# Kernel optimization log

Measured on AMD Instinct MI355X. Metric: run time of the kernel, lower is better.

## Reference

```python
import jax, jax.numpy as jnp
import numpy as np


def setup_inputs() -> dict:
    key = jax.random.key(0)
    k1, k2, k3, k4 = jax.random.split(key, 4)
    N, M, d = 512, 4096, 8
    return {
        "X": jax.random.normal(k1, (N, M), jnp.float32),
        "C_tilde": jax.random.normal(k2, (d, N), jnp.float32),
        "S_tilde": jax.random.normal(k3, (N, d), jnp.float32),
        "tau_tilde": jax.random.normal(k4, (N, d), jnp.float32),
    }


def reference(X, C_tilde, S_tilde, tau_tilde):
    # X: [N, M] real; C_tilde: [d, N]; S_tilde, tau_tilde: [N, d]
    N, M = X.shape
    f = jnp.arange(M, dtype=X.dtype) / M                         # [M]
    # omega[N,d,M] = exp(-2*pi*i * tau[N,d] * f[M])
    phase = tau_tilde[:, :, None] * f                            # [N, d, M] real
    omega = jnp.exp((-2j * jnp.pi) * phase.astype(jnp.complex64))  # [N, d, M] complex64

    X_F = jnp.fft.fft(X)                                         # [N, M] complex64
    X_F_align = X_F[:, None, :] * jnp.conj(omega)                # [N, d, M]

    C = jax.nn.softmax(C_tilde, axis=1).astype(jnp.complex64)    # [d, N]
    A_F = jnp.einsum('dN,NdM->dM', C, X_F_align)                 # [d, M]

    S = jax.nn.softmax(S_tilde, axis=1).astype(jnp.complex64)    # [N, d]
    # S_shift[N,d,M] = S[N,d] * omega[N,d,M]; x = sum_d S_shift * A_F
    x = jnp.einsum('Nd,NdM,dM->NM', S, omega, A_F)               # [N, M] complex64
    return x
```

## Files before the change

### kernel.cpp

```cpp
#include <hip/hip_runtime.h>
#include <math.h>

#define N_ROWS 512
#define M_LEN  4096
#define D_DIM  8
#define NCHUNK 8

__device__ __forceinline__ float2 f2(float x, float y) { return make_float2(x, y); }
__device__ __forceinline__ float2 cmul(float2 a, float2 b){
  return f2(a.x*b.x - a.y*b.y, a.x*b.y + a.y*b.x);
}
__device__ __forceinline__ float2 cadd(float2 a, float2 b){ return f2(a.x+b.x, a.y+b.y); }
__device__ __forceinline__ float2 csub(float2 a, float2 b){ return f2(a.x-b.x, a.y-b.y); }
__device__ __forceinline__ int ph(int i){ return i + (i>>4) + (i>>8); }
__device__ __forceinline__ int dr6(int j){
  int r = 0;
  #pragma unroll
  for (int i = 0; i < 6; ++i){ r = (r<<2) | (j & 3); j >>= 2; }
  return r;
}

static constexpr float TWO_PI = 6.283185307179586476925f;

__global__ __launch_bounds__(256) void softmax_kernel(
    const float* __restrict__ Ct, const float* __restrict__ St,
    float* __restrict__ C, float* __restrict__ S) {
  int b = blockIdx.x, tid = threadIdx.x;
  if (b < D_DIM) {
    __shared__ float red[256];
    const float* row = Ct + b * N_ROWS;
    float v0 = row[tid], v1 = row[tid + 256];
    float mx = fmaxf(v0, v1);
    red[tid] = mx; __syncthreads();
    for (int s = 128; s > 0; s >>= 1) {
      if (tid < s) red[tid] = fmaxf(red[tid], red[tid + s]);
      __syncthreads();
    }
    float m = red[0];
    __syncthreads();
    float e0 = __expf(v0 - m), e1 = __expf(v1 - m);
    red[tid] = e0 + e1; __syncthreads();
    for (int s = 128; s > 0; s >>= 1) {
      if (tid < s) red[tid] += red[tid + s];
      __syncthreads();
    }
    float inv = 1.0f / red[0];
    C[b * N_ROWS + tid]       = e0 * inv;
    C[b * N_ROWS + tid + 256] = e1 * inv;
  } else {
    int n = (b - D_DIM) * 256 + tid;
    if (n < N_ROWS) {
      float v[D_DIM];
      float mx = -3.0e38f;
      #pragma unroll
      for (int d = 0; d < D_DIM; ++d) { v[d] = St[n * D_DIM + d]; mx = fmaxf(mx, v[d]); }
      float sum = 0.f;
      #pragma unroll
      for (int d = 0; d < D_DIM; ++d) { v[d] = __expf(v[d] - mx); sum += v[d]; }
      float inv = 1.0f / sum;
      #pragma unroll
      for (int d = 0; d < D_DIM; ++d) S[n * D_DIM + d] = v[d] * inv;
    }
  }
}

__global__ __launch_bounds__(256) void fft_kernel(
    const float* __restrict__ X, float2* __restrict__ XF) {
  __shared__ float2 buf[4368];
  int row = blockIdx.x;
  int tid = threadIdx.x;
  const float* x = X + (size_t)row * M_LEN;
  for (int j = tid; j < M_LEN; j += 256)
    buf[ph(dr6(j))] = f2(x[j], 0.0f);
  __syncthreads();
  for (int s = 0; s < 6; ++s) {
    int quarter = 1 << (2*s);
    float angf = -TWO_PI / (float)(quarter << 2);
    for (int bi = tid; bi < 1024; bi += 256) {
      int k  = bi & (quarter - 1);
      int g  = bi >> (2*s);
      int i0 = (g << (2*s + 2)) + k;
      float sw, cw; __sincosf(angf * (float)k, &sw, &cw);
      float2 w1 = f2(cw, sw);
      float2 w2 = cmul(w1, w1);
      float2 w3 = cmul(w2, w1);
      float2 a0 = buf[ph(i0)];
      float2 a1 = cmul(buf[ph(i0 +   quarter)], w1);
      float2 a2 = cmul(buf[ph(i0 + 2*quarter)], w2);
      float2 a3 = cmul(buf[ph(i0 + 3*quarter)], w3);
      float2 t0 = cadd(a0, a2), t1 = csub(a0, a2);
      float2 t2 = cadd(a1, a3), t3 = csub(a1, a3);
      buf[ph(i0)]             = cadd(t0, t2);
      buf[ph(i0 +   quarter)] = f2(t1.x + t3.y, t1.y - t3.x);
      buf[ph(i0 + 2*quarter)] = csub(t0, t2);
      buf[ph(i0 + 3*quarter)] = f2(t1.x - t3.y, t1.y + t3.x);
    }
    __syncthreads();
  }
  for (int j = tid; j < M_LEN; j += 256)
    XF[(size_t)row * M_LEN + j] = buf[ph(j)];
}

__global__ __launch_bounds__(256) void zero_af_kernel(float4* __restrict__ AF) {
  int i = blockIdx.x * 256 + threadIdx.x;
  if (i < (D_DIM * M_LEN) / 2)
    AF[i] = make_float4(0.f, 0.f, 0.f, 0.f);
}

__global__ __launch_bounds__(256) void af_kernel(
    const float2* __restrict__ XF, const float* __restrict__ C,
    const float* __restrict__ tau, float* __restrict__ AF) {
  int bid   = blockIdx.x;
  int chunk = bid >> 7;
  int idx   = (bid & 127) * 256 + threadIdx.x;
  int d = idx >> 12;
  int m = idx & (M_LEN - 1);
  float fm = (float)m * (1.0f / (float)M_LEN);
  float accr = 0.f, acci = 0.f;
  int n0 = chunk * (N_ROWS / NCHUNK);
  #pragma unroll 8
  for (int nn = 0; nn < N_ROWS / NCHUNK; ++nn) {
    int n = n0 + nn;
    float c = C[d * N_ROWS + n];
    float t = tau[n * D_DIM + d];
    float sa, ca;
    __sincosf(TWO_PI * t * fm, &sa, &ca);
    float2 Xv = XF[(size_t)n * M_LEN + m];
    accr += c * (Xv.x * ca - Xv.y * sa);
    acci += c * (Xv.x * sa + Xv.y * ca);
  }
  if (idx < D_DIM * M_LEN) {
    atomicAdd(&AF[2 * idx],     accr);
    atomicAdd(&AF[2 * idx + 1], acci);
  }
}

__global__ __launch_bounds__(256) void out_kernel(
    const float2* __restrict__ AF, const float* __restrict__ S,
    const float* __restrict__ tau, float* __restrict__ out, int interleaved) {
  int idx = blockIdx.x * 256 + threadIdx.x;
  int n = idx >> 12;
  int m = idx & (M_LEN - 1);
  float fm = (float)m * (1.0f / (float)M_LEN);
  float xr = 0.f, xi = 0.f;
  #pragma unroll
  for (int d = 0; d < D_DIM; ++d) {
    float s = S[n * D_DIM + d];
    float t = tau[n * D_DIM + d];
    float sa, ca;
    __sincosf(TWO_PI * t * fm, &sa, &ca);
    float2 A = AF[(d << 12) + m];
    xr += s * (ca * A.x + sa * A.y);
    xi += s * (ca * A.y - sa * A.x);
  }
  if (interleaved) {
    ((float2*)out)[idx] = f2(xr, xi);
  } else {
    out[idx] = xr;
  }
}

extern "C" void kernel_launch(void* const* d_in, const int* in_sizes, int n_in,
                              void* d_out, int out_size, void* d_ws, size_t ws_size,
                              hipStream_t stream) {
  const float* X  = (const float*)d_in[0];
  const float* Ct = (const float*)d_in[1];
  const float* St = (const float*)d_in[2];
  const float* tau= (const float*)d_in[3];

  char* ws = (char*)d_ws;
  const size_t XF_BYTES = (size_t)N_ROWS * M_LEN * sizeof(float2);
  const size_t AF_BYTES = (size_t)D_DIM * M_LEN * sizeof(float2);
  const size_t C_BYTES  = (size_t)D_DIM * N_ROWS * sizeof(float);
  float2* XF = (float2*)ws;
  float2* AF = (float2*)(ws + XF_BYTES);
  float*  C  = (float*)(ws + XF_BYTES + AF_BYTES);
  float*  S  = (float*)(ws + XF_BYTES + AF_BYTES + C_BYTES);

  int interleaved = (out_size >= 2 * N_ROWS * M_LEN) ? 1 : 0;

  softmax_kernel<<<D_DIM + (N_ROWS + 255) / 256, 256, 0, stream>>>(Ct, St, C, S);
  fft_kernel<<<N_ROWS, 256, 0, stream>>>(X, XF);
  zero_af_kernel<<<(D_DIM * M_LEN / 2 + 255) / 256, 256, 0, stream>>>((float4*)AF);
  af_kernel<<<NCHUNK * 128, 256, 0, stream>>>(XF, C, tau, (float*)AF);
  out_kernel<<<(N_ROWS * M_LEN) / 256, 256, 0, stream>>>(AF, S, tau, (float*)d_out, interleaved);
}
```

Before: 115.2 us.

## Reuse XF loads across all d in af_kernel and use revolution-based hardware sin/cos

The A_F accumulation now has each thread own one frequency m and keep 8 accumulators, one per d. Each XF element is therefore loaded once per n instead of once per (n,d), which cuts global traffic on the large XF buffer by a factor of eight. The N split grows from 8 to 32 chunks so the grid still fills the device, at the cost of more atomics. All sin/cos calls switch to AMD's native v_sin/v_cos builtins, which take angles in revolutions, so the 2*pi multiply and range reduction are dropped. The risk is lower accuracy for large arguments.

```diff
diff --git a/kernel.cpp b/kernel.cpp
--- a/kernel.cpp
+++ b/kernel.cpp
@@ -4,7 +4,7 @@
 #define N_ROWS 512
 #define M_LEN  4096
 #define D_DIM  8
-#define NCHUNK 8
+#define NCHUNK 32
 
 __device__ __forceinline__ float2 f2(float x, float y) { return make_float2(x, y); }
 __device__ __forceinline__ float2 cmul(float2 a, float2 b){
@@ -19,8 +19,8 @@
   for (int i = 0; i < 6; ++i){ r = (r<<2) | (j & 3); j >>= 2; }
   return r;
 }
-
-static constexpr float TWO_PI = 6.283185307179586476925f;
+__device__ __forceinline__ float sin_rev(float x){ return __builtin_amdgcn_sinf(x); }
+__device__ __forceinline__ float cos_rev(float x){ return __builtin_amdgcn_cosf(x); }
 
 __global__ __launch_bounds__(256) void softmax_kernel(
     const float* __restrict__ Ct, const float* __restrict__ St,
@@ -75,12 +75,13 @@
   __syncthreads();
   for (int s = 0; s < 6; ++s) {
     int quarter = 1 << (2*s);
-    float angf = -TWO_PI / (float)(quarter << 2);
+    float negInv = -1.0f / (float)(quarter << 2);
     for (int bi = tid; bi < 1024; bi += 256) {
       int k  = bi & (quarter - 1);
       int g  = bi >> (2*s);
       int i0 = (g << (2*s + 2)) + k;
-      float sw, cw; __sincosf(angf * (float)k, &sw, &cw);
+      float rev = negInv * (float)k;
+      float sw = sin_rev(rev), cw = cos_rev(rev);
       float2 w1 = f2(cw, sw);
       float2 w2 = cmul(w1, w1);
       float2 w3 = cmul(w2, w1);
@@ -111,27 +112,31 @@
     const float2* __restrict__ XF, const float* __restrict__ C,
     const float* __restrict__ tau, float* __restrict__ AF) {
   int bid   = blockIdx.x;
-  int chunk = bid >> 7;
-  int idx   = (bid & 127) * 256 + threadIdx.x;
-  int d = idx >> 12;
-  int m = idx & (M_LEN - 1);
-  float fm = (float)m * (1.0f / (float)M_LEN);
-  float accr = 0.f, acci = 0.f;
+  int chunk = bid >> 4;
+  int m     = (bid & 15) * 256 + threadIdx.x;
+  float fm  = (float)m * (1.0f / (float)M_LEN);
+  float accr[D_DIM], acci[D_DIM];
+  #pragma unroll
+  for (int d = 0; d < D_DIM; ++d) { accr[d] = 0.f; acci[d] = 0.f; }
   int n0 = chunk * (N_ROWS / NCHUNK);
-  #pragma unroll 8
+  #pragma unroll 4
   for (int nn = 0; nn < N_ROWS / NCHUNK; ++nn) {
     int n = n0 + nn;
-    float c = C[d * N_ROWS + n];
-    float t = tau[n * D_DIM + d];
-    float sa, ca;
-    __sincosf(TWO_PI * t * fm, &sa, &ca);
     float2 Xv = XF[(size_t)n * M_LEN + m];
-    accr += c * (Xv.x * ca - Xv.y * sa);
-    acci += c * (Xv.x * sa + Xv.y * ca);
+    #pragma unroll
+    for (int d = 0; d < D_DIM; ++d) {
+      float t = tau[n * D_DIM + d];
+      float c = C[d * N_ROWS + n];
+      float r = t * fm;
+      float s_ = sin_rev(r), c_ = cos_rev(r);
+      accr[d] += c * (Xv.x * c_ - Xv.y * s_);
+      acci[d] += c * (Xv.x * s_ + Xv.y * c_);
+    }
   }
-  if (idx < D_DIM * M_LEN) {
-    atomicAdd(&AF[2 * idx],     accr);
-    atomicAdd(&AF[2 * idx + 1], acci);
+  #pragma unroll
+  for (int d = 0; d < D_DIM; ++d) {
+    atomicAdd(&AF[2 * ((d << 12) + m)],     accr[d]);
+    atomicAdd(&AF[2 * ((d << 12) + m) + 1], acci[d]);
   }
 }
 
@@ -147,8 +152,8 @@
   for (int d = 0; d < D_DIM; ++d) {
     float s = S[n * D_DIM + d];
     float t = tau[n * D_DIM + d];
-    float sa, ca;
-    __sincosf(TWO_PI * t * fm, &sa, &ca);
+    float r = t * fm;
+    float sa = sin_rev(r), ca = cos_rev(r);
     float2 A = AF[(d << 12) + m];
     xr += s * (ca * A.x + sa * A.y);
     xi += s * (ca * A.y - sa * A.x);
@@ -182,6 +187,6 @@
   softmax_kernel<<<D_DIM + (N_ROWS + 255) / 256, 256, 0, stream>>>(Ct, St, C, S);
   fft_kernel<<<N_ROWS, 256, 0, stream>>>(X, XF);
   zero_af_kernel<<<(D_DIM * M_LEN / 2 + 255) / 256, 256, 0, stream>>>((float4*)AF);
-  af_kernel<<<NCHUNK * 128, 256, 0, stream>>>(XF, C, tau, (float*)AF);
+  af_kernel<<<NCHUNK * 16, 256, 0, stream>>>(XF, C, tau, (float*)AF);
   out_kernel<<<(N_ROWS * M_LEN) / 256, 256, 0, stream>>>(AF, S, tau, (float*)d_out, interleaved);
 }
```

New measurement: 121.3 us. 5.3% more time.
